# Kernel tuning notes

Hardware: AMD Instinct MI355X
Metric: run time of the kernel (lower is better)

The kernel has to match this reference:

```python
import jax, jax.numpy as jnp
import numpy as np

WIN = 7
K1, K2 = 0.01, 0.03
NP_ = WIN * WIN
COV_NORM = NP_ / (NP_ - 1)


def _box_conv(x, w):
    return jax.lax.conv_general_dilated(
        x, w, window_strides=(1, 1), padding='VALID',
        dimension_numbers=('NCHW', 'OIHW', 'NCHW'))


def setup_inputs() -> dict:
    key = jax.random.key(0)
    k1, k2 = jax.random.split(key)
    B, C, H, W = 64, 2, 320, 320
    X = jax.random.uniform(k1, (B, C, H, W), dtype=jnp.float32)
    Y = jax.random.uniform(k2, (B, C, H, W), dtype=jnp.float32)
    data_range = jnp.ones((B, 1, 1, 1), dtype=jnp.float32)
    w = jnp.ones((1, C, WIN, WIN), dtype=jnp.float32) / (WIN * WIN)
    return {"X": X, "Y": Y, "data_range": data_range, "w": w}


def reference(X, Y, data_range, w):
    C1 = (K1 * data_range) ** 2
    C2 = (K2 * data_range) ** 2
    ux = _box_conv(X, w)
    uy = _box_conv(Y, w)
    uxx = _box_conv(X * X, w)
    uyy = _box_conv(Y * Y, w)
    uxy = _box_conv(X * Y, w)
    vx = COV_NORM * (uxx - ux * ux)
    vy = COV_NORM * (uyy - uy * uy)
    vxy = COV_NORM * (uxy - ux * uy)
    A1 = 2 * ux * uy + C1
    A2 = 2 * vxy + C2
    B1 = ux ** 2 + uy ** 2 + C1
    B2 = vx + vy + C2
    S = (A1 * A2) / (B1 * B2)
    return 1 - S.mean()
```

## Files before the change

kernel.cpp:

```cpp
#include <hip/hip_runtime.h>

#define WW 320
#define OWID 314
#define OHEI 314
#define BB 64
#define RPB 28
#define NBAND 12
#define NSTRIP 79
#define NTH 256
#define NBLK ((BB * NBAND * NSTRIP) / NTH)

__device__ __forceinline__ void load_row(
    const float* __restrict__ X0, const float* __restrict__ X1,
    const float* __restrict__ Y0, const float* __restrict__ Y1,
    int off, int o2, float4 r4[8], float2 r2[4])
{
    r4[0] = *(const float4*)(X0 + off);
    r4[1] = *(const float4*)(X0 + off + 4);
    r2[0] = *(const float2*)(X0 + off + o2);
    r4[2] = *(const float4*)(X1 + off);
    r4[3] = *(const float4*)(X1 + off + 4);
    r2[1] = *(const float2*)(X1 + off + o2);
    r4[4] = *(const float4*)(Y0 + off);
    r4[5] = *(const float4*)(Y0 + off + 4);
    r2[2] = *(const float2*)(Y0 + off + o2);
    r4[6] = *(const float4*)(Y1 + off);
    r4[7] = *(const float4*)(Y1 + off + 4);
    r2[3] = *(const float2*)(Y1 + off + o2);
}

__device__ __forceinline__ void math_row(const float4 r4[8], const float2 r2[4], float h[20])
{
    float x0[10] = {r4[0].x, r4[0].y, r4[0].z, r4[0].w, r4[1].x, r4[1].y, r4[1].z, r4[1].w, r2[0].x, r2[0].y};
    float x1[10] = {r4[2].x, r4[2].y, r4[2].z, r4[2].w, r4[3].x, r4[3].y, r4[3].z, r4[3].w, r2[1].x, r2[1].y};
    float y0[10] = {r4[4].x, r4[4].y, r4[4].z, r4[4].w, r4[5].x, r4[5].y, r4[5].z, r4[5].w, r2[2].x, r2[2].y};
    float y1[10] = {r4[6].x, r4[6].y, r4[6].z, r4[6].w, r4[7].x, r4[7].y, r4[7].z, r4[7].w, r2[3].x, r2[3].y};

    float sx[10], sy[10], sxx[10], syy[10], sxy[10];
    #pragma unroll
    for (int j = 0; j < 10; ++j) {
        sx[j]  = x0[j] + x1[j];
        sy[j]  = y0[j] + y1[j];
        sxx[j] = x0[j] * x0[j] + x1[j] * x1[j];
        syy[j] = y0[j] * y0[j] + y1[j] * y1[j];
        sxy[j] = x0[j] * y0[j] + x1[j] * y1[j];
    }
    #pragma unroll
    for (int q = 0; q < 5; ++q) {
        const float* m = (q == 0) ? sx : (q == 1) ? sy : (q == 2) ? sxx : (q == 3) ? syy : sxy;
        float t0 = ((m[0] + m[1]) + (m[2] + m[3])) + ((m[4] + m[5]) + m[6]);
        float t1 = t0 - m[0] + m[7];
        float t2 = t1 - m[1] + m[8];
        float t3 = t2 - m[2] + m[9];
        h[q * 4 + 0] = t0; h[q * 4 + 1] = t1; h[q * 4 + 2] = t2; h[q * 4 + 3] = t3;
    }
}

__global__ __launch_bounds__(NTH, 1) void ssim_main(
    const float* __restrict__ X, const float* __restrict__ Y,
    const float* __restrict__ dr, double* __restrict__ acc,
    unsigned* __restrict__ counter, float* __restrict__ out)
{
    const int wi   = blockIdx.x * NTH + threadIdx.x;
    const int s    = wi % NSTRIP;
    const int g    = wi / NSTRIP;
    const int band = g % NBAND;
    const int b    = g / NBAND;
    const int r0   = band * RPB;
    const int cb   = s * 4;
    const int o2   = (cb <= 308) ? 8 : 4;

    const size_t plane = (size_t)WW * WW;
    const float* X0 = X + (size_t)b * 2 * plane;
    const float* X1 = X0 + plane;
    const float* Y0 = Y + (size_t)b * 2 * plane;
    const float* Y1 = Y0 + plane;

    const float d  = dr[b];
    const float C1 = (0.01f * d) * (0.01f * d);
    const float C2 = (0.03f * d) * (0.03f * d);

    float cm[4];
    #pragma unroll
    for (int j = 0; j < 4; ++j) cm[j] = (cb + j < OWID) ? 1.0f : 0.0f;

    float ring[7][20];
    #pragma unroll
    for (int k = 0; k < 7; ++k)
        #pragma unroll
        for (int q = 0; q < 20; ++q) ring[k][q] = 0.0f;

    float v[20];
    #pragma unroll
    for (int q = 0; q < 20; ++q) v[q] = 0.0f;

    float4 c4[8], n4[8];
    float2 c2[4], n2[4];
    load_row(X0, X1, Y0, Y1, r0 * WW + cb, o2, c4, c2);

    float ssum = 0.0f;
    const float inv = 1.0f / 49.0f;
    const float cn  = 49.0f / 48.0f;

    for (int i7 = 0; i7 < 35; i7 += 7) {
        #pragma unroll
        for (int k = 0; k < 7; ++k) {
            const int i = i7 + k;

            if (i < 33) {
                const int rn = min(r0 + i + 1, WW - 1);
                load_row(X0, X1, Y0, Y1, rn * WW + cb, o2, n4, n2);
            }
            if (i < 34) {
                float h[20];
                math_row(c4, c2, h);
                #pragma unroll
                for (int q = 0; q < 20; ++q) {
                    v[q] += h[q] - ring[k][q];
                    ring[k][q] = h[q];
                }

                const int t = r0 + i - 6;
                if (i >= 6 && t < OHEI) {
                    #pragma unroll
                    for (int j = 0; j < 4; ++j) {
                        float ux  = v[j]      * inv, uy  = v[4 + j]  * inv;
                        float uxx = v[8 + j]  * inv, uyy = v[12 + j] * inv, uxy = v[16 + j] * inv;
                        float vx  = cn * (uxx - ux * ux);
                        float vy  = cn * (uyy - uy * uy);
                        float vxy = cn * (uxy - ux * uy);
                        float A1  = 2.0f * ux * uy + C1;
                        float A2  = 2.0f * vxy + C2;
                        float B1  = ux * ux + uy * uy + C1;
                        float B2  = vx + vy + C2;
                        ssum += cm[j] * (A1 * A2) / (B1 * B2);
                    }
                }

                #pragma unroll
                for (int q = 0; q < 8; ++q) c4[q] = n4[q];
                #pragma unroll
                for (int q = 0; q < 4; ++q) c2[q] = n2[q];
            }
        }
    }

    double local = (double)ssum;
    #pragma unroll
    for (int off = 32; off > 0; off >>= 1)
        local += __shfl_down(local, off, 64);
    __shared__ double wsum[NTH / 64];
    const int lane = threadIdx.x & 63, wid = threadIdx.x >> 6;
    if (lane == 0) wsum[wid] = local;
    __syncthreads();
    if (threadIdx.x == 0) {
        double tot = (wsum[0] + wsum[1]) + (wsum[2] + wsum[3]);
        atomicAdd(acc, tot);
        __threadfence();
        unsigned ticket = atomicAdd(counter, 1u);
        if (ticket == NBLK - 1) {
            double stot = atomicAdd(acc, 0.0);
            const double N = (double)BB * (double)OHEI * (double)OWID;
            out[0] = (float)(1.0 - stot / N);
        }
    }
}

extern "C" void kernel_launch(void* const* d_in, const int* in_sizes, int n_in,
                              void* d_out, int out_size, void* d_ws, size_t ws_size,
                              hipStream_t stream)
{
    const float* X  = (const float*)d_in[0];
    const float* Y  = (const float*)d_in[1];
    const float* dr = (const float*)d_in[2];
    double*   acc     = (double*)d_ws;
    unsigned* counter = (unsigned*)((char*)d_ws + 8);
    float*    out     = (float*)d_out;

    hipMemsetAsync(d_ws, 0, 16, stream);
    ssim_main<<<dim3(NBLK), dim3(NTH), 0, stream>>>(X, Y, dr, acc, counter, out);
}
```

Measured before the change: 141.4 us.

## Move sliding-window ring to LDS and deepen row prefetch to two rows

Moves the 7x20 per-thread horizontal-sum ring from registers into shared memory, read and written as float4 per thread. It deepens the row prefetch from one row to two using a triple-buffered register set, and fully unrolls the 34-row loop. The aim is to free VGPRs (the ring alone took 140) so loads can run further ahead and latency is better hidden. The cost is LDS traffic on every row, large LDS use per block (about 140KB for 256 threads), and much more code from the full unroll.

Result: slower. 281.0 us (+98.8%).

```diff
diff --git a/kernel.cpp b/kernel.cpp
--- a/kernel.cpp
+++ b/kernel.cpp
@@ -7,6 +7,7 @@
 #define RPB 28
 #define NBAND 12
 #define NSTRIP 79
+#define NROWS (RPB + 6)
 #define NTH 256
 #define NBLK ((BB * NBAND * NSTRIP) / NTH)
 
@@ -61,6 +62,8 @@
     const float* __restrict__ dr, double* __restrict__ acc,
     unsigned* __restrict__ counter, float* __restrict__ out)
 {
+    __shared__ float ring[7][NTH][20];
+
     const int wi   = blockIdx.x * NTH + threadIdx.x;
     const int s    = wi % NSTRIP;
     const int g    = wi / NSTRIP;
@@ -84,63 +87,69 @@
     #pragma unroll
     for (int j = 0; j < 4; ++j) cm[j] = (cb + j < OWID) ? 1.0f : 0.0f;
 
-    float ring[7][20];
-    #pragma unroll
-    for (int k = 0; k < 7; ++k)
-        #pragma unroll
-        for (int q = 0; q < 20; ++q) ring[k][q] = 0.0f;
-
     float v[20];
     #pragma unroll
     for (int q = 0; q < 20; ++q) v[q] = 0.0f;
 
-    float4 c4[8], n4[8];
-    float2 c2[4], n2[4];
-    load_row(X0, X1, Y0, Y1, r0 * WW + cb, o2, c4, c2);
+    float4 b4[3][8];
+    float2 b2[3][4];
+    load_row(X0, X1, Y0, Y1, r0 * WW + cb, o2, b4[0], b2[0]);
+    {
+        const int rn = min(r0 + 1, WW - 1);
+        load_row(X0, X1, Y0, Y1, rn * WW + cb, o2, b4[1], b2[1]);
+    }
 
     float ssum = 0.0f;
     const float inv = 1.0f / 49.0f;
     const float cn  = 49.0f / 48.0f;
+    float* const myring = &ring[0][threadIdx.x][0];
 
-    for (int i7 = 0; i7 < 35; i7 += 7) {
-        #pragma unroll
-        for (int k = 0; k < 7; ++k) {
-            const int i = i7 + k;
+    #pragma unroll
+    for (int i = 0; i < NROWS; ++i) {
+        if (i + 2 < NROWS) {
+            const int rn = min(r0 + i + 2, WW - 1);
+            load_row(X0, X1, Y0, Y1, rn * WW + cb, o2, b4[(i + 2) % 3], b2[(i + 2) % 3]);
+        }
 
-            if (i < 33) {
-                const int rn = min(r0 + i + 1, WW - 1);
-                load_row(X0, X1, Y0, Y1, rn * WW + cb, o2, n4, n2);
-            }
-            if (i < 34) {
-                float h[20];
-                math_row(c4, c2, h);
+        float h[20];
+        math_row(b4[i % 3], b2[i % 3], h);
+
+        float* rp = myring + (i % 7) * (NTH * 20);
+
+        if (i >= 7) {
+            float ro[20];
+            #pragma unroll
+            for (int q = 0; q < 5; ++q)
+                *(float4*)&ro[4 * q] = *(const float4*)&rp[4 * q];
+            #pragma unroll
+            for (int q = 0; q < 20; ++q) v[q] += h[q] - ro[q];
+        } else {
+            #pragma unroll
+            for (int q = 0; q < 20; ++q) v[q] += h[q];
+        }
+
+        if (i < NROWS - 7) {
+            #pragma unroll
+            for (int q = 0; q < 5; ++q)
+                *(float4*)&rp[4 * q] = *(const float4*)&h[4 * q];
+        }
+
+        if (i >= 6) {
+            const int t = r0 + i - 6;
+            if (t < OHEI) {
                 #pragma unroll
-                for (int q = 0; q < 20; ++q) {
-                    v[q] += h[q] - ring[k][q];
-                    ring[k][q] = h[q];
+                for (int j = 0; j < 4; ++j) {
+                    float ux  = v[j]      * inv, uy  = v[4 + j]  * inv;
+                    float uxx = v[8 + j]  * inv, uyy = v[12 + j] * inv, uxy = v[16 + j] * inv;
+                    float vx  = cn * (uxx - ux * ux);
+                    float vy  = cn * (uyy - uy * uy);
+                    float vxy = cn * (uxy - ux * uy);
+                    float A1  = 2.0f * ux * uy + C1;
+                    float A2  = 2.0f * vxy + C2;
+                    float B1  = ux * ux + uy * uy + C1;
+                    float B2  = vx + vy + C2;
+                    ssum += cm[j] * (A1 * A2) / (B1 * B2);
                 }
-
-                const int t = r0 + i - 6;
-                if (i >= 6 && t < OHEI) {
-                    #pragma unroll
-                    for (int j = 0; j < 4; ++j) {
-                        float ux  = v[j]      * inv, uy  = v[4 + j]  * inv;
-                        float uxx = v[8 + j]  * inv, uyy = v[12 + j] * inv, uxy = v[16 + j] * inv;
-                        float vx  = cn * (uxx - ux * ux);
-                        float vy  = cn * (uyy - uy * uy);
-                        float vxy = cn * (uxy - ux * uy);
-                        float A1  = 2.0f * ux * uy + C1;
-                        float A2  = 2.0f * vxy + C2;
-                        float B1  = ux * ux + uy * uy + C1;
-                        float B2  = vx + vy + C2;
-                        ssum += cm[j] * (A1 * A2) / (B1 * B2);
-                    }
-                }
-
-                #pragma unroll
-                for (int q = 0; q < 8; ++q) c4[q] = n4[q];
-                #pragma unroll
-                for (int q = 0; q < 4; ++q) c2[q] = n2[q];
             }
         }
     }
```
